# Optimization experiments

Hardware: AMD Instinct MI355X
Metric: run time of the kernel (lower is better)

The kernel has to match this reference:

```python
import jax, jax.numpy as jnp
import numpy as np

K = 1  # BaseSnapFunction.k default

def setup_inputs() -> dict:
    key = jax.random.key(0)
    k1, k2 = jax.random.split(key)
    B, S, D = 4, 2048, 1024
    C, N = 16, 2048          # num_codebooks, num_codes
    x = jax.random.normal(k1, (B, S, D), dtype=jnp.float32)
    codebook = jax.random.normal(k2, (C, N, D // C), dtype=jnp.float32)
    return {"x": x, "codebook": codebook}

def reference(x, codebook):
    B, S, D = x.shape
    C, N, sub = codebook.shape
    xr = x.reshape(B, S, C, sub)                      # split dim into C chunks
    # squared euclidean distance (monotone in true distance -> same argmin)
    dots = jnp.einsum('bscd,cnd->bscn', xr, codebook)  # [B,S,C,N]
    xsq = jnp.sum(xr * xr, axis=-1)                    # [B,S,C]
    cbsq = jnp.sum(codebook * codebook, axis=-1)       # [C,N]
    d2 = xsq[..., None] - 2.0 * dots + cbsq[None, None]
    idx = jnp.argmin(d2, axis=-1)                      # [B,S,C], k=1 topk of -dist
    # gather per-codebook features and concat chunks back to dim
    quant = codebook[jnp.arange(C)[None, None, :], idx]  # [B,S,C,sub]
    out = quant.reshape(B, S, D) / K
    return out
```

## Files before the change

### kernel.cpp

```cpp
#include <hip/hip_runtime.h>

constexpr int BS    = 8192;
constexpr int CCH   = 16;
constexpr int NCODE = 2048;

using s16x8 = __attribute__((ext_vector_type(8))) short;
using f32x4 = __attribute__((ext_vector_type(4))) float;


__device__ __forceinline__ unsigned short bf16_rne(float v) {
    unsigned u = __float_as_uint(v);
    return (unsigned short)((u + 0x7fffu + ((u >> 16) & 1u)) >> 16);
}
__device__ __forceinline__ void split1(float v, unsigned short& h, unsigned short& l) {
    h = bf16_rne(v);
    const float hf = __uint_as_float((unsigned)h << 16);
    l = bf16_rne(v - hf);
}
__device__ __forceinline__ void split4(float4 v, ushort4& h, ushort4& l) {
    split1(v.x, h.x, l.x); split1(v.y, h.y, l.y);
    split1(v.z, h.z, l.z); split1(v.w, h.w, l.w);
}
__device__ __forceinline__ unsigned enc_f(float s) {
    unsigned u = __float_as_uint(s);
    return (u & 0x80000000u) ? ~u : (u | 0x80000000u);
}

__device__ __forceinline__ s16x8 ldfrag(const char* buf, int row, int ke) {
    return *(const s16x8*)(buf + row * 128 + ((((ke >> 3) ^ row) & 7) * 16));
}

__device__ __forceinline__ void gload16(const void* g, void* l) {
    __builtin_amdgcn_global_load_lds(
        (const __attribute__((address_space(1))) void*)g,
        (__attribute__((address_space(3))) void*)l, 16, 0, 0);
}

__device__ __forceinline__ void merge2(float& b1, int& bi, float& b2,
                                       float ob1, int obi, float ob2) {
    b2 = fminf(fminf(b2, ob2), fmaxf(b1, ob1));
    if (ob1 < b1 || (ob1 == b1 && obi < bi)) { b1 = ob1; bi = obi; }
}

__global__ void cbsq_kernel(const float* __restrict__ cb, float* __restrict__ cbsq,
                            float* __restrict__ cmax)
{
    const int g = blockIdx.x * 256 + threadIdx.x;
    const float4* cg = (const float4*)cb;
    float s = 0.f;
#pragma unroll
    for (int q = 0; q < 16; ++q) {
        float4 v = cg[(size_t)g * 16 + q];
        s = fmaf(v.x, v.x, s); s = fmaf(v.y, v.y, s);
        s = fmaf(v.z, v.z, s); s = fmaf(v.w, v.w, s);
    }
    cbsq[g] = s;
    atomicMax((unsigned*)cmax, __float_as_uint(s));
}

__global__ void presplit_cb(const float* __restrict__ cb,
                            unsigned short* __restrict__ cbh,
                            unsigned short* __restrict__ cbl)
{
    const int g = blockIdx.x * 256 + threadIdx.x;
    const float4 v = ((const float4*)cb)[g];
    ushort4 h, l; split4(v, h, l);
    ((ushort4*)cbh)[g] = h;
    ((ushort4*)cbl)[g] = l;
}

__global__ __launch_bounds__(256, 2)
void vq_fp32_fallback(const float* __restrict__ x, const float* __restrict__ cb,
                      float* __restrict__ out)
{
    __shared__ __align__(16) char smraw[65536];
    float4 (*xs)[128] = reinterpret_cast<float4(*)[128]>(smraw);
    float4 (*cs)[128] = reinterpret_cast<float4(*)[128]>(smraw + 32768);
    float  (*rs)[128] = reinterpret_cast<float(*)[128]>(smraw);
    int    (*ri)[128] = reinterpret_cast<int(*)[128]>(smraw + 8192);
    int    *bfin      = reinterpret_cast<int*>(smraw + 16384);

    const int tid = threadIdx.x, tx = tid & 15, ty = tid >> 4;
    const int c = blockIdx.y, mbase = blockIdx.x * 128;
    const float4* xg = (const float4*)x;
    const float4* cg = (const float4*)cb;
    {
        const int k4 = tid & 15, mrow0 = tid >> 4;
#pragma unroll
        for (int i = 0; i < 8; ++i) {
            const int m = i * 16 + mrow0;
            xs[k4][m] = xg[(size_t)(mbase + m) * 256 + c * 16 + k4];
        }
    }
    float best[8]; int bidx[8];
#pragma unroll
    for (int ii = 0; ii < 8; ++ii) { best[ii] = 3.4e38f; bidx[ii] = 0; }
    for (int nt = 0; nt < 16; ++nt) {
        __syncthreads();
        {
            const int k4 = tid & 15, nrow0 = tid >> 4;
#pragma unroll
            for (int i = 0; i < 8; ++i) {
                const int n = i * 16 + nrow0;
                cs[k4][n] = cg[((size_t)c * NCODE + nt * 128 + n) * 16 + k4];
            }
        }
        __syncthreads();
        float acc[8][8], csq[8];
#pragma unroll
        for (int ii = 0; ii < 8; ++ii)
#pragma unroll
            for (int jj = 0; jj < 8; ++jj) acc[ii][jj] = 0.f;
#pragma unroll
        for (int jj = 0; jj < 8; ++jj) csq[jj] = 0.f;
#pragma unroll 2
        for (int k4 = 0; k4 < 16; ++k4) {
            float4 xv[8], cv[8];
#pragma unroll
            for (int ii = 0; ii < 8; ++ii) xv[ii] = xs[k4][tx + 16 * ii];
#pragma unroll
            for (int jj = 0; jj < 8; ++jj) cv[jj] = cs[k4][ty + 16 * jj];
#pragma unroll
            for (int jj = 0; jj < 8; ++jj) {
                csq[jj] = fmaf(cv[jj].x, cv[jj].x, csq[jj]);
                csq[jj] = fmaf(cv[jj].y, cv[jj].y, csq[jj]);
                csq[jj] = fmaf(cv[jj].z, cv[jj].z, csq[jj]);
                csq[jj] = fmaf(cv[jj].w, cv[jj].w, csq[jj]);
            }
#pragma unroll
            for (int ii = 0; ii < 8; ++ii)
#pragma unroll
                for (int jj = 0; jj < 8; ++jj) {
                    acc[ii][jj] = fmaf(xv[ii].x, cv[jj].x, acc[ii][jj]);
                    acc[ii][jj] = fmaf(xv[ii].y, cv[jj].y, acc[ii][jj]);
                    acc[ii][jj] = fmaf(xv[ii].z, cv[jj].z, acc[ii][jj]);
                    acc[ii][jj] = fmaf(xv[ii].w, cv[jj].w, acc[ii][jj]);
                }
        }
#pragma unroll
        for (int jj = 0; jj < 8; ++jj) {
            const int n = nt * 128 + ty + 16 * jj;
#pragma unroll
            for (int ii = 0; ii < 8; ++ii) {
                const float s = fmaf(-2.f, acc[ii][jj], csq[jj]);
                if (s < best[ii]) { best[ii] = s; bidx[ii] = n; }
            }
        }
    }
    __syncthreads();
#pragma unroll
    for (int ii = 0; ii < 8; ++ii) {
        const int m = tx + 16 * ii;
        rs[ty][m] = best[ii]; ri[ty][m] = bidx[ii];
    }
    __syncthreads();
    if (tid < 128) {
        float b = rs[0][tid]; int bi = ri[0][tid];
#pragma unroll
        for (int j = 1; j < 16; ++j) {
            const float s = rs[j][tid]; const int i2 = ri[j][tid];
            if (s < b || (s == b && i2 < bi)) { b = s; bi = i2; }
        }
        bfin[tid] = bi;
    }
    __syncthreads();
    {
        float4* og = (float4*)out;
#pragma unroll
        for (int i = 0; i < 8; ++i) {
            const int flat = i * 256 + tid, m = flat >> 4, q = flat & 15;
            og[(size_t)(mbase + m) * 256 + c * 16 + q] =
                cg[((size_t)c * NCODE + bfin[m]) * 16 + q];
        }
    }
}

template<bool PRESPLIT>
__global__ __launch_bounds__(256, 2)
void pass1(const float* __restrict__ x, const float* __restrict__ cb,
           const unsigned short* __restrict__ cbh, const unsigned short* __restrict__ cbl,
           const float* __restrict__ cbsq, const float* __restrict__ cmax,
           float* __restrict__ out, int* __restrict__ bcnt, int* __restrict__ bwl,
           unsigned long long* __restrict__ pbest)
{
    __shared__ __align__(1024) char sm[65536];
    const int tid  = threadIdx.x;
    const int lane = tid & 63, wv = tid >> 6;
    const int l15  = lane & 15, quad = lane >> 4;
    const int c = blockIdx.y, mbase = blockIdx.x * 128;
    const float4* xg = (const float4*)x;
    const float4* cg = (const float4*)cb;
    const float cmaxs = sqrtf(*cmax);
    const int cwb = (wv & 1) * 64, tkb = (wv >> 1) * 64;

    int tdec[4], ndec[4];
    {
        char* calV = sm;
        char* calO = sm + 16384;
#pragma unroll
        for (int i = 0; i < 8; ++i) {
            const int flat = i * 256 + tid, row = flat >> 4, f4c = flat & 15;
            const int off = row * 128 + ((((f4c >> 1) ^ row) & 7) * 16) + (f4c & 1) * 8;
            const unsigned short hv = bf16_rne((float)(row & 15));
            const unsigned short ho = bf16_rne(1.0f);
            ushort4 v4 = {hv, hv, hv, hv}, o4 = {ho, ho, ho, ho};
            *(ushort4*)(calV + off) = v4;
            *(ushort4*)(calO + off) = o4;
        }
        __syncthreads();
        const int ke = quad * 8;
        const s16x8 aV = ldfrag(calV, cwb + l15, ke);
        const s16x8 aO = ldfrag(calO, cwb + l15, ke);
        const s16x8 bV = ldfrag(calV, tkb + l15, ke);
        const s16x8 bO = ldfrag(calO, tkb + l15, ke);
        f32x4 z; z[0] = z[1] = z[2] = z[3] = 0.f;
        const f32x4 at = __builtin_amdgcn_mfma_f32_16x16x32_bf16(aO, bV, z, 0, 0, 0);
        const f32x4 an = __builtin_amdgcn_mfma_f32_16x16x32_bf16(aV, bO, z, 0, 0, 0);
#pragma unroll
        for (int r = 0; r < 4; ++r) {
            tdec[r] = ((int)(at[r] + 0.5f) >> 5) & 15;
            ndec[r] = ((int)(an[r] + 0.5f) >> 5) & 15;
        }
        __syncthreads();
    }

    char* xs_hi = sm;
    char* xs_lo = sm + 16384;
    {
        float4 xf[8];
#pragma unroll
        for (int i = 0; i < 8; ++i) {
            const int flat = i * 256 + tid;
            xf[i] = xg[(size_t)(mbase + (flat >> 4)) * 256 + c * 16 + (flat & 15)];
        }
#pragma unroll
        for (int i = 0; i < 8; ++i) {
            const int flat = i * 256 + tid, row = flat >> 4, f4c = flat & 15;
            ushort4 h, l; split4(xf[i], h, l);
            const int off = row * 128 + ((((f4c >> 1) ^ row) & 7) * 16) + (f4c & 1) * 8;
            *(ushort4*)(xs_hi + off) = h;
            *(ushort4*)(xs_lo + off) = l;
        }
    }
    __syncthreads();

    s16x8 bhf[4][2], blf[4][2];
#pragma unroll
    for (int jt = 0; jt < 4; ++jt)
#pragma unroll
        for (int ks = 0; ks < 2; ++ks) {
            const int rowt = tkb + jt * 16 + l15;
            const int ke = ks * 32 + quad * 8;
            bhf[jt][ks] = ldfrag(xs_hi, rowt, ke);
            blf[jt][ks] = ldfrag(xs_lo, rowt, ke);
        }

    float4 pf[8];
    uint4  ph[4], pl[4];
    if (PRESPLIT) {
        const uint4* sh = (const uint4*)(cbh + (size_t)c * NCODE * 64);
        const uint4* sl = (const uint4*)(cbl + (size_t)c * NCODE * 64);
#pragma unroll
        for (int i = 0; i < 4; ++i) {
            const int flat = i * 256 + tid;
            ph[i] = sh[flat]; pl[i] = sl[flat];
        }
    } else {
        const float4* src = cg + (size_t)c * NCODE * 16;
#pragma unroll
        for (int i = 0; i < 8; ++i) {
            const int flat = i * 256 + tid;
            pf[i] = src[(size_t)(flat >> 4) * 16 + (flat & 15)];
        }
    }

    float s1[4][4], s2[4][4]; int i1[4][4];
#pragma unroll
    for (int jt = 0; jt < 4; ++jt)
#pragma unroll
        for (int r = 0; r < 4; ++r) { s1[jt][r] = 3.4e38f; s2[jt][r] = 3.4e38f; i1[jt][r] = 0; }

    for (int nt = 0; nt < 16; ++nt) {
        char* chi = (nt & 1) ? sm : sm + 32768;
        char* clo = chi + 16384;
        if (PRESPLIT) {
#pragma unroll
            for (int i = 0; i < 4; ++i) {
                const int flat = i * 256 + tid;
                const int row = flat >> 3, ch = flat & 7;
                const int phys = (ch ^ row) & 7;
                *(uint4*)(chi + row * 128 + phys * 16) = ph[i];
                *(uint4*)(clo + row * 128 + phys * 16) = pl[i];
            }
        } else {
#pragma unroll
            for (int i = 0; i < 8; ++i) {
                const int flat = i * 256 + tid, row = flat >> 4, f4c = flat & 15;
                ushort4 h, l; split4(pf[i], h, l);
                const int off = row * 128 + ((((f4c >> 1) ^ row) & 7) * 16) + (f4c & 1) * 8;
                *(ushort4*)(chi + off) = h;
                *(ushort4*)(clo + off) = l;
            }
        }
        __syncthreads();
        if (nt < 15) {
            if (PRESPLIT) {
                const uint4* sh = (const uint4*)(cbh + ((size_t)c * NCODE + (nt + 1) * 128) * 64);
                const uint4* sl = (const uint4*)(cbl + ((size_t)c * NCODE + (nt + 1) * 128) * 64);
#pragma unroll
                for (int i = 0; i < 4; ++i) {
                    const int flat = i * 256 + tid;
                    ph[i] = sh[flat]; pl[i] = sl[flat];
                }
            } else {
                const float4* src = cg + ((size_t)c * NCODE + (nt + 1) * 128) * 16;
#pragma unroll
                for (int i = 0; i < 8; ++i) {
                    const int flat = i * 256 + tid;
                    pf[i] = src[(size_t)(flat >> 4) * 16 + (flat & 15)];
                }
            }
        }
        const float* cbn = cbsq + c * NCODE + nt * 128;
        float csqv[4][4];
#pragma unroll
        for (int mt = 0; mt < 4; ++mt)
#pragma unroll
            for (int r = 0; r < 4; ++r)
                csqv[mt][r] = cbn[cwb + mt * 16 + ndec[r]];

#pragma unroll
        for (int mt = 0; mt < 4; ++mt) {
            f32x4 accj[4];
#pragma unroll
            for (int jt = 0; jt < 4; ++jt)
#pragma unroll
                for (int e = 0; e < 4; ++e) accj[jt][e] = 0.f;
#pragma unroll
            for (int ks = 0; ks < 2; ++ks) {
                const int ke = ks * 32 + quad * 8;
                const int rowc = cwb + mt * 16 + l15;
                const s16x8 ah = ldfrag(chi, rowc, ke);
                const s16x8 al = ldfrag(clo, rowc, ke);
#pragma unroll
                for (int jt = 0; jt < 4; ++jt) {
                    accj[jt] = __builtin_amdgcn_mfma_f32_16x16x32_bf16(ah, bhf[jt][ks], accj[jt], 0, 0, 0);
                    accj[jt] = __builtin_amdgcn_mfma_f32_16x16x32_bf16(ah, blf[jt][ks], accj[jt], 0, 0, 0);
                    accj[jt] = __builtin_amdgcn_mfma_f32_16x16x32_bf16(al, bhf[jt][ks], accj[jt], 0, 0, 0);
                }
            }
#pragma unroll
            for (int jt = 0; jt < 4; ++jt)
#pragma unroll
                for (int r = 0; r < 4; ++r) {
                    const float s = fmaf(-2.f, accj[jt][r], csqv[mt][r]);
                    const int n = nt * 128 + cwb + mt * 16 + ndec[r];
                    const bool lt = s < s1[jt][r];
                    s2[jt][r] = fminf(s2[jt][r], fmaxf(s, s1[jt][r]));
                    i1[jt][r] = lt ? n : i1[jt][r];
                    s1[jt][r] = fminf(s1[jt][r], s);
                }
        }
    }

    __syncthreads();
    float* s1a = (float*)sm;
    int*   i1a = (int*)(sm + 16384);
    float* s2a = (float*)(sm + 32768);
    float* sm_part = (float*)(sm + 49152);
    int*   bfin    = (int*)(sm + 57344);
#pragma unroll
    for (int jt = 0; jt < 4; ++jt)
#pragma unroll
        for (int r = 0; r < 4; ++r) {
            const int tok = tkb + jt * 16 + tdec[r];
            const int idx = tok * 32 + (wv & 1) * 16 + ndec[r];
            s1a[idx] = s1[jt][r]; i1a[idx] = i1[jt][r]; s2a[idx] = s2[jt][r];
        }
    {
        const float4* src = xg + (size_t)mbase * 256 + c * 16;
#pragma unroll
        for (int i = 0; i < 8; ++i) {
            const int flat = i * 256 + tid, row = flat >> 4, f4c = flat & 15;
            const float4 v = src[(size_t)row * 256 + f4c];
            sm_part[row * 16 + f4c] = v.x * v.x + v.y * v.y + v.z * v.z + v.w * v.w;
        }
    }
    __syncthreads();
    if (tid < 128) {
        float b1 = 3.4e38f, b2 = 3.4e38f; int bi = 0;
#pragma unroll 4
        for (int e = 0; e < 32; ++e) {
            const float se = s1a[tid * 32 + e];
            const int   ie = i1a[tid * 32 + e];
            const float s2e = s2a[tid * 32 + e];
            if (se < b1 || (se == b1 && ie < bi)) { b2 = fminf(b2, b1); b1 = se; bi = ie; }
            else b2 = fminf(b2, se);
            b2 = fminf(b2, s2e);
        }
        float xsq = 0.f;
#pragma unroll
        for (int q = 0; q < 16; ++q) xsq += sm_part[tid * 16 + q];
        const float eps = 3e-4f + 2e-4f * sqrtf(xsq) * cmaxs;
        bfin[tid] = bi;
        if (b2 - b1 <= 2.f * eps) {
            const int slot = atomicAdd(&bcnt[c], 1);
            bwl[c * 8192 + slot] = mbase + tid;
            pbest[c * 8192 + slot] = ~0ULL;
        }
    }
    __syncthreads();
    {
        float4* og = (float4*)out;
#pragma unroll
        for (int i = 0; i < 8; ++i) {
            const int flat = i * 256 + tid, m = flat >> 4, q = flat & 15;
            og[(size_t)(mbase + m) * 256 + c * 16 + q] =
                cg[((size_t)c * NCODE + bfin[m]) * 16 + q];
        }
    }
}

__global__ __launch_bounds__(256, 2)
void pass1_gl(const float* __restrict__ x, const float* __restrict__ cb,
              const unsigned short* __restrict__ cbh, const unsigned short* __restrict__ cbl,
              const float* __restrict__ cbsq, const float* __restrict__ cmax,
              float* __restrict__ out, int* __restrict__ bcnt, int* __restrict__ bwl,
              unsigned long long* __restrict__ pbest)
{
    __shared__ __align__(1024) char sm[65536];
    const int tid  = threadIdx.x;
    const int lane = tid & 63, wv = tid >> 6;
    const int l15  = lane & 15, quad = lane >> 4;
    const int c = blockIdx.y, mbase = blockIdx.x * 128;
    const float4* xg = (const float4*)x;
    const float4* cg = (const float4*)cb;
    const float cmaxs = sqrtf(*cmax);
    const int cwb = (wv & 1) * 64, tkb = (wv >> 1) * 64;

    char* bufA = sm;
    char* bufB = sm + 32768;

    const int lanebyte = ((lane >> 3) << 7) | ((((lane & 7) ^ (lane >> 3)) & 7) << 4);
    const char* srcH = (const char*)cbh + (size_t)c * NCODE * 128;
    const char* srcL = (const char*)cbl + (size_t)c * NCODE * 128;
    const int wchunk = wv * 4096;

#pragma unroll
    for (int j = 0; j < 4; ++j) {
        const int o = wchunk + j * 1024;
        gload16(srcH + o + lanebyte, bufB + o);
        gload16(srcL + o + lanebyte, bufB + 16384 + o);
    }
    float4 xf[8];
#pragma unroll
    for (int i = 0; i < 8; ++i) {
        const int flat = i * 256 + tid;
        xf[i] = xg[(size_t)(mbase + (flat >> 4)) * 256 + c * 16 + (flat & 15)];
    }

    int tdec[4], ndec[4];
    {
        const short one = (short)bf16_rne(1.0f);
        const short val = (short)bf16_rne((float)l15);
        s16x8 aV, aO;
#pragma unroll
        for (int e = 0; e < 8; ++e) { aV[e] = val; aO[e] = one; }
        f32x4 z; z[0] = z[1] = z[2] = z[3] = 0.f;
        const f32x4 at = __builtin_amdgcn_mfma_f32_16x16x32_bf16(aO, aV, z, 0, 0, 0);
        const f32x4 an = __builtin_amdgcn_mfma_f32_16x16x32_bf16(aV, aO, z, 0, 0, 0);
#pragma unroll
        for (int r = 0; r < 4; ++r) {
            tdec[r] = ((int)(at[r] + 0.5f) >> 5) & 15;
            ndec[r] = ((int)(an[r] + 0.5f) >> 5) & 15;
        }
    }

    float p8[8];
#pragma unroll
    for (int i = 0; i < 8; ++i) {
        const int flat = i * 256 + tid, row = flat >> 4, f4c = flat & 15;
        ushort4 h, l; split4(xf[i], h, l);
        const int off = row * 128 + ((((f4c >> 1) ^ row) & 7) * 16) + (f4c & 1) * 8;
        *(ushort4*)(bufA + off) = h;
        *(ushort4*)(bufA + 16384 + off) = l;
        p8[i] = xf[i].x * xf[i].x + xf[i].y * xf[i].y + xf[i].z * xf[i].z + xf[i].w * xf[i].w;
    }
    __syncthreads();

    s16x8 bhf[4][2], blf[4][2];
#pragma unroll
    for (int jt = 0; jt < 4; ++jt)
#pragma unroll
        for (int ks = 0; ks < 2; ++ks) {
            const int rowt = tkb + jt * 16 + l15;
            const int ke = ks * 32 + quad * 8;
            bhf[jt][ks] = ldfrag(bufA, rowt, ke);
            blf[jt][ks] = ldfrag(bufA + 16384, rowt, ke);
        }
    __syncthreads();

    float s1[4][4], s2[4][4]; int i1[4][4];
#pragma unroll
    for (int jt = 0; jt < 4; ++jt)
#pragma unroll
        for (int r = 0; r < 4; ++r) { s1[jt][r] = 3.4e38f; s2[jt][r] = 3.4e38f; i1[jt][r] = 0; }

    for (int nt = 0; nt < 16; ++nt) {
        char* chi = (nt & 1) ? bufA : bufB;
        char* clo = chi + 16384;

        const float* cbn = cbsq + c * NCODE + nt * 128;
        float csqv[4][4];
#pragma unroll
        for (int mt = 0; mt < 4; ++mt)
#pragma unroll
            for (int r = 0; r < 4; ++r)
                csqv[mt][r] = cbn[cwb + mt * 16 + ndec[r]];
        asm volatile("" ::: "memory");

        if (nt < 15) {
            char* nh = (nt & 1) ? bufB : bufA;
            const char* th = srcH + (size_t)(nt + 1) * 16384;
            const char* tl = srcL + (size_t)(nt + 1) * 16384;
#pragma unroll
            for (int j = 0; j < 4; ++j) {
                const int o = wchunk + j * 1024;
                gload16(th + o + lanebyte, nh + o);
                gload16(tl + o + lanebyte, nh + 16384 + o);
            }
        }

#pragma unroll
        for (int mt = 0; mt < 4; ++mt) {
            f32x4 accj[4];
#pragma unroll
            for (int jt = 0; jt < 4; ++jt)
#pragma unroll
                for (int e = 0; e < 4; ++e) accj[jt][e] = 0.f;
#pragma unroll
            for (int ks = 0; ks < 2; ++ks) {
                const int ke = ks * 32 + quad * 8;
                const int rowc = cwb + mt * 16 + l15;
                const s16x8 ah = ldfrag(chi, rowc, ke);
                const s16x8 al = ldfrag(clo, rowc, ke);
#pragma unroll
                for (int jt = 0; jt < 4; ++jt) {
                    accj[jt] = __builtin_amdgcn_mfma_f32_16x16x32_bf16(ah, bhf[jt][ks], accj[jt], 0, 0, 0);
                    accj[jt] = __builtin_amdgcn_mfma_f32_16x16x32_bf16(ah, blf[jt][ks], accj[jt], 0, 0, 0);
                    accj[jt] = __builtin_amdgcn_mfma_f32_16x16x32_bf16(al, bhf[jt][ks], accj[jt], 0, 0, 0);
                }
            }
#pragma unroll
            for (int jt = 0; jt < 4; ++jt)
#pragma unroll
                for (int r = 0; r < 4; ++r) {
                    const float s = fmaf(-2.f, accj[jt][r], csqv[mt][r]);
                    const int n = nt * 128 + cwb + mt * 16 + ndec[r];
                    const bool lt = s < s1[jt][r];
                    s2[jt][r] = fminf(s2[jt][r], fmaxf(s, s1[jt][r]));
                    i1[jt][r] = lt ? n : i1[jt][r];
                    s1[jt][r] = fminf(s1[jt][r], s);
                }
        }
        __syncthreads();
    }

    float* s1h = (float*)sm;
    int*   i1h = (int*)  (sm + 1024);
    float* s2h = (float*)(sm + 2048);
    float* xsq_l = (float*)(sm + 3072);
    int*   bfin  = (int*)  (sm + 3584);

#pragma unroll
    for (int jt = 0; jt < 4; ++jt) {
        float b1 = s1[jt][0], b2 = s2[jt][0]; int bi = i1[jt][0];
#pragma unroll
        for (int r = 1; r < 4; ++r)
            merge2(b1, bi, b2, s1[jt][r], i1[jt][r], s2[jt][r]);
#pragma unroll
        for (int m = 16; m <= 32; m <<= 1) {
            const float ob1 = __shfl_xor(b1, m);
            const int   obi = __shfl_xor(bi, m);
            const float ob2 = __shfl_xor(b2, m);
            merge2(b1, bi, b2, ob1, obi, ob2);
        }
        if (quad == 0) {
            const int tok = tkb + jt * 16 + tdec[0];
            s1h[tok * 2 + (wv & 1)] = b1;
            i1h[tok * 2 + (wv & 1)] = bi;
            s2h[tok * 2 + (wv & 1)] = b2;
        }
    }
#pragma unroll
    for (int i = 0; i < 8; ++i) {
        float v = p8[i];
        v += __shfl_xor(v, 1); v += __shfl_xor(v, 2);
        v += __shfl_xor(v, 4); v += __shfl_xor(v, 8);
        if (l15 == 0) xsq_l[i * 16 + (tid >> 4)] = v;
    }
    __syncthreads();
    if (tid < 128) {
        float b1 = s1h[tid * 2], b2 = s2h[tid * 2]; int bi = i1h[tid * 2];
        merge2(b1, bi, b2, s1h[tid * 2 + 1], i1h[tid * 2 + 1], s2h[tid * 2 + 1]);
        const float xsq = xsq_l[tid];
        const float eps = 3e-4f + 2e-4f * sqrtf(xsq) * cmaxs;
        bfin[tid] = bi;
        if (b2 - b1 <= 2.f * eps) {
            const int slot = atomicAdd(&bcnt[c], 1);
            bwl[c * 8192 + slot] = mbase + tid;
            pbest[c * 8192 + slot] = ~0ULL;
        }
    }
    __syncthreads();
    {
        float4* og = (float4*)out;
#pragma unroll
        for (int i = 0; i < 8; ++i) {
            const int flat = i * 256 + tid, m = flat >> 4, q = flat & 15;
            og[(size_t)(mbase + m) * 256 + c * 16 + q] =
                cg[((size_t)c * NCODE + bfin[m]) * 16 + q];
        }
    }
}

__global__ __launch_bounds__(256, 2)
void pass2_nt(const float* __restrict__ x, const float* __restrict__ cb,
              const int* __restrict__ bcnt, const int* __restrict__ bwl,
              unsigned long long* __restrict__ pbest)
{
    __shared__ __align__(16) char smraw[65536];
    __shared__ int toks[128];
    float4 (*xs)[128] = reinterpret_cast<float4(*)[128]>(smraw);
    float4 (*cs)[128] = reinterpret_cast<float4(*)[128]>(smraw + 32768);
    float  (*rs)[128] = reinterpret_cast<float(*)[128]>(smraw);
    int    (*ri)[128] = reinterpret_cast<int(*)[128]>(smraw + 8192);

    const int c = blockIdx.y, ntb = blockIdx.x;
    const int cnt = bcnt[c];
    if (cnt == 0) return;
    const int tid = threadIdx.x, tx = tid & 15, ty = tid >> 4;
    const float4* xg = (const float4*)x;
    const float4* cg = (const float4*)cb;

    {
        const int k4 = tid & 15, nrow0 = tid >> 4;
#pragma unroll
        for (int i = 0; i < 8; ++i) {
            const int n = i * 16 + nrow0;
            cs[k4][n] = cg[((size_t)c * NCODE + ntb * 128 + n) * 16 + k4];
        }
    }

    for (int g0 = 0; g0 < cnt; g0 += 128) {
        __syncthreads();
        if (tid < 128) {
            const int e = g0 + tid;
            toks[tid] = bwl[c * 8192 + (e < cnt ? e : g0)];
        }
        __syncthreads();
        {
            const int k4 = tid & 15, mrow0 = tid >> 4;
#pragma unroll
            for (int i = 0; i < 8; ++i) {
                const int m = i * 16 + mrow0;
                xs[k4][m] = xg[(size_t)toks[m] * 256 + c * 16 + k4];
            }
        }
        __syncthreads();
        float acc[8][8], csq[8];
#pragma unroll
        for (int ii = 0; ii < 8; ++ii)
#pragma unroll
            for (int jj = 0; jj < 8; ++jj) acc[ii][jj] = 0.f;
#pragma unroll
        for (int jj = 0; jj < 8; ++jj) csq[jj] = 0.f;
#pragma unroll 2
        for (int k4 = 0; k4 < 16; ++k4) {
            float4 xv[8], cv[8];
#pragma unroll
            for (int ii = 0; ii < 8; ++ii) xv[ii] = xs[k4][tx + 16 * ii];
#pragma unroll
            for (int jj = 0; jj < 8; ++jj) cv[jj] = cs[k4][ty + 16 * jj];
#pragma unroll
            for (int jj = 0; jj < 8; ++jj) {
                csq[jj] = fmaf(cv[jj].x, cv[jj].x, csq[jj]);
                csq[jj] = fmaf(cv[jj].y, cv[jj].y, csq[jj]);
                csq[jj] = fmaf(cv[jj].z, cv[jj].z, csq[jj]);
                csq[jj] = fmaf(cv[jj].w, cv[jj].w, csq[jj]);
            }
#pragma unroll
            for (int ii = 0; ii < 8; ++ii)
#pragma unroll
                for (int jj = 0; jj < 8; ++jj) {
                    acc[ii][jj] = fmaf(xv[ii].x, cv[jj].x, acc[ii][jj]);
                    acc[ii][jj] = fmaf(xv[ii].y, cv[jj].y, acc[ii][jj]);
                    acc[ii][jj] = fmaf(xv[ii].z, cv[jj].z, acc[ii][jj]);
                    acc[ii][jj] = fmaf(xv[ii].w, cv[jj].w, acc[ii][jj]);
                }
        }
        float best[8]; int bidx[8];
#pragma unroll
        for (int ii = 0; ii < 8; ++ii) { best[ii] = 3.4e38f; bidx[ii] = 0; }
#pragma unroll
        for (int jj = 0; jj < 8; ++jj) {
            const int n = ntb * 128 + ty + 16 * jj;
#pragma unroll
            for (int ii = 0; ii < 8; ++ii) {
                const float s = fmaf(-2.f, acc[ii][jj], csq[jj]);
                if (s < best[ii]) { best[ii] = s; bidx[ii] = n; }
            }
        }
        __syncthreads();
#pragma unroll
        for (int ii = 0; ii < 8; ++ii) {
            const int m = tx + 16 * ii;
            rs[ty][m] = best[ii]; ri[ty][m] = bidx[ii];
        }
        __syncthreads();
        if (tid < 128 && g0 + tid < cnt) {
            float b = rs[0][tid]; int bi = ri[0][tid];
#pragma unroll
            for (int j = 1; j < 16; ++j) {
                const float s = rs[j][tid]; const int i2 = ri[j][tid];
                if (s < b || (s == b && i2 < bi)) { b = s; bi = i2; }
            }
            const unsigned long long pk =
                ((unsigned long long)enc_f(b) << 32) | (unsigned)bi;
            atomicMin(&pbest[c * 8192 + g0 + tid], pk);
        }
    }
}

__global__ void pass3(const float* __restrict__ cb, float* __restrict__ out,
                      const int* __restrict__ bcnt, const int* __restrict__ bwl,
                      const unsigned long long* __restrict__ pbest)
{
    const int c = blockIdx.y;
    const int cnt = bcnt[c];
    const float4* cg = (const float4*)cb;
    float4* og = (float4*)out;
    const int q = threadIdx.x & 15;
    for (int e = blockIdx.x * 16 + (threadIdx.x >> 4); e < cnt; e += 64 * 16) {
        const int tok = bwl[c * 8192 + e];
        const unsigned n = (unsigned)(pbest[c * 8192 + e] & 0xFFFFFFFFull);
        og[(size_t)tok * 256 + c * 16 + q] = cg[((size_t)c * NCODE + n) * 16 + q];
    }
}

extern "C" void kernel_launch(void* const* d_in, const int* in_sizes, int n_in,
                              void* d_out, int out_size, void* d_ws, size_t ws_size,
                              hipStream_t stream)
{
    const float* x  = (const float*)d_in[0];
    const float* cb = (const float*)d_in[1];
    float* out      = (float*)d_out;

    if (ws_size < (size_t)(2u << 20)) {
        dim3 grid(BS / 128, CCH);
        vq_fp32_fallback<<<grid, 256, 0, stream>>>(x, cb, out);
        return;
    }
    char* ws = (char*)d_ws;
    float* cbsq = (float*)ws;
    float* cmax = (float*)(ws + 131072);
    int*   bcnt = (int*)(ws + 131076);
    int*   bwl  = (int*)(ws + 131328);
    unsigned long long* pbest = (unsigned long long*)(ws + 655616);
    unsigned short* cbh = (unsigned short*)(ws + (2u << 20));
    unsigned short* cbl = (unsigned short*)(ws + (6u << 20));

    hipMemsetAsync(ws + 131072, 0, 68, stream);
    cbsq_kernel<<<CCH * NCODE / 256, 256, 0, stream>>>(cb, cbsq, cmax);
    if (ws_size >= (size_t)(10u << 20)) {
        presplit_cb<<<2048, 256, 0, stream>>>(cb, cbh, cbl);
        pass1_gl<<<dim3(BS / 128, CCH), 256, 0, stream>>>(x, cb, cbh, cbl, cbsq, cmax, out, bcnt, bwl, pbest);
    } else {
        pass1<false><<<dim3(BS / 128, CCH), 256, 0, stream>>>(x, cb, nullptr, nullptr, cbsq, cmax, out, bcnt, bwl, pbest);
    }
    pass2_nt<<<dim3(16, CCH), 256, 0, stream>>>(x, cb, bcnt, bwl, pbest);
    pass3<<<dim3(64, CCH), 256, 0, stream>>>(cb, out, bcnt, bwl, pbest);
}
```

Measured before the change: 228.7 us.

## Fuse codebook prep kernels and split pass1 work across eight waves

Merges the codebook squared-norm kernel and the bf16 hi/lo presplit kernel into a single prep kernel that reads each float4 once and reduces the norms with lane shuffles, removing one launch and one full read of the codebook. The main pass1 kernel now runs 512 threads (8 waves) per block instead of 256. Each wave handles 32 codes instead of 64 and does half the loads, and the per-token best/second-best merge now spans four wave partitions. This raises parallelism per block and cuts per-thread register use, at the cost of more LDS reduction traffic and a possible occupancy limit from 64KB of shared memory per block.

Result: slower. 758.8 us (+231.8%).

```diff
diff --git a/kernel.cpp b/kernel.cpp
--- a/kernel.cpp
+++ b/kernel.cpp
@@ -42,31 +42,25 @@
     if (ob1 < b1 || (ob1 == b1 && obi < bi)) { b1 = ob1; bi = obi; }
 }
 
-__global__ void cbsq_kernel(const float* __restrict__ cb, float* __restrict__ cbsq,
-                            float* __restrict__ cmax)
-{
-    const int g = blockIdx.x * 256 + threadIdx.x;
-    const float4* cg = (const float4*)cb;
-    float s = 0.f;
-#pragma unroll
-    for (int q = 0; q < 16; ++q) {
-        float4 v = cg[(size_t)g * 16 + q];
-        s = fmaf(v.x, v.x, s); s = fmaf(v.y, v.y, s);
-        s = fmaf(v.z, v.z, s); s = fmaf(v.w, v.w, s);
-    }
-    cbsq[g] = s;
-    atomicMax((unsigned*)cmax, __float_as_uint(s));
-}
-
-__global__ void presplit_cb(const float* __restrict__ cb,
-                            unsigned short* __restrict__ cbh,
-                            unsigned short* __restrict__ cbl)
+template<bool SPLIT>
+__global__ void prep(const float* __restrict__ cb, float* __restrict__ cbsq,
+                     float* __restrict__ cmax,
+                     unsigned short* __restrict__ cbh, unsigned short* __restrict__ cbl)
 {
     const int g = blockIdx.x * 256 + threadIdx.x;
     const float4 v = ((const float4*)cb)[g];
-    ushort4 h, l; split4(v, h, l);
-    ((ushort4*)cbh)[g] = h;
-    ((ushort4*)cbl)[g] = l;
+    if (SPLIT) {
+        ushort4 h, l; split4(v, h, l);
+        ((ushort4*)cbh)[g] = h;
+        ((ushort4*)cbl)[g] = l;
+    }
+    float s = v.x * v.x + v.y * v.y + v.z * v.z + v.w * v.w;
+    s += __shfl_xor(s, 1); s += __shfl_xor(s, 2);
+    s += __shfl_xor(s, 4); s += __shfl_xor(s, 8);
+    if ((threadIdx.x & 15) == 0) {
+        cbsq[g >> 4] = s;
+        atomicMax((unsigned*)cmax, __float_as_uint(s));
+    }
 }
 
 __global__ __launch_bounds__(256, 2)
@@ -421,12 +415,12 @@
     }
 }
 
-__global__ __launch_bounds__(256, 2)
-void pass1_gl(const float* __restrict__ x, const float* __restrict__ cb,
-              const unsigned short* __restrict__ cbh, const unsigned short* __restrict__ cbl,
-              const float* __restrict__ cbsq, const float* __restrict__ cmax,
-              float* __restrict__ out, int* __restrict__ bcnt, int* __restrict__ bwl,
-              unsigned long long* __restrict__ pbest)
+__global__ __launch_bounds__(512, 4)
+void pass1_gl8(const float* __restrict__ x, const float* __restrict__ cb,
+               const unsigned short* __restrict__ cbh, const unsigned short* __restrict__ cbl,
+               const float* __restrict__ cbsq, const float* __restrict__ cmax,
+               float* __restrict__ out, int* __restrict__ bcnt, int* __restrict__ bwl,
+               unsigned long long* __restrict__ pbest)
 {
     __shared__ __align__(1024) char sm[65536];
     const int tid  = threadIdx.x;
@@ -436,7 +430,8 @@
     const float4* xg = (const float4*)x;
     const float4* cg = (const float4*)cb;
     const float cmaxs = sqrtf(*cmax);
-    const int cwb = (wv & 1) * 64, tkb = (wv >> 1) * 64;
+    const int cwb = (wv & 3) * 32;
+    const int tkb = (wv >> 2) * 64;
 
     char* bufA = sm;
     char* bufB = sm + 32768;
@@ -444,18 +439,18 @@
     const int lanebyte = ((lane >> 3) << 7) | ((((lane & 7) ^ (lane >> 3)) & 7) << 4);
     const char* srcH = (const char*)cbh + (size_t)c * NCODE * 128;
     const char* srcL = (const char*)cbl + (size_t)c * NCODE * 128;
-    const int wchunk = wv * 4096;
-
-#pragma unroll
-    for (int j = 0; j < 4; ++j) {
+    const int wchunk = wv * 2048;
+
+#pragma unroll
+    for (int j = 0; j < 2; ++j) {
         const int o = wchunk + j * 1024;
         gload16(srcH + o + lanebyte, bufB + o);
         gload16(srcL + o + lanebyte, bufB + 16384 + o);
     }
-    float4 xf[8];
-#pragma unroll
-    for (int i = 0; i < 8; ++i) {
-        const int flat = i * 256 + tid;
+    float4 xf[4];
+#pragma unroll
+    for (int i = 0; i < 4; ++i) {
+        const int flat = i * 512 + tid;
         xf[i] = xg[(size_t)(mbase + (flat >> 4)) * 256 + c * 16 + (flat & 15)];
     }
 
@@ -476,15 +471,15 @@
         }
     }
 
-    float p8[8];
-#pragma unroll
-    for (int i = 0; i < 8; ++i) {
-        const int flat = i * 256 + tid, row = flat >> 4, f4c = flat & 15;
+    float p4[4];
+#pragma unroll
+    for (int i = 0; i < 4; ++i) {
+        const int flat = i * 512 + tid, row = flat >> 4, f4c = flat & 15;
         ushort4 h, l; split4(xf[i], h, l);
         const int off = row * 128 + ((((f4c >> 1) ^ row) & 7) * 16) + (f4c & 1) * 8;
         *(ushort4*)(bufA + off) = h;
         *(ushort4*)(bufA + 16384 + off) = l;
-        p8[i] = xf[i].x * xf[i].x + xf[i].y * xf[i].y + xf[i].z * xf[i].z + xf[i].w * xf[i].w;
+        p4[i] = xf[i].x * xf[i].x + xf[i].y * xf[i].y + xf[i].z * xf[i].z + xf[i].w * xf[i].w;
     }
     __syncthreads();
 
@@ -511,9 +506,9 @@
         char* clo = chi + 16384;
 
         const float* cbn = cbsq + c * NCODE + nt * 128;
-        float csqv[4][4];
-#pragma unroll
-        for (int mt = 0; mt < 4; ++mt)
+        float csqv[2][4];
+#pragma unroll
+        for (int mt = 0; mt < 2; ++mt)
 #pragma unroll
             for (int r = 0; r < 4; ++r)
                 csqv[mt][r] = cbn[cwb + mt * 16 + ndec[r]];
@@ -524,7 +519,7 @@
             const char* th = srcH + (size_t)(nt + 1) * 16384;
             const char* tl = srcL + (size_t)(nt + 1) * 16384;
 #pragma unroll
-            for (int j = 0; j < 4; ++j) {
+            for (int j = 0; j < 2; ++j) {
                 const int o = wchunk + j * 1024;
                 gload16(th + o + lanebyte, nh + o);
                 gload16(tl + o + lanebyte, nh + 16384 + o);
@@ -532,7 +527,7 @@
         }
 
 #pragma unroll
-        for (int mt = 0; mt < 4; ++mt) {
+        for (int mt = 0; mt < 2; ++mt) {
             f32x4 accj[4];
 #pragma unroll
             for (int jt = 0; jt < 4; ++jt)
@@ -567,10 +562,10 @@
     }
 
     float* s1h = (float*)sm;
-    int*   i1h = (int*)  (sm + 1024);
-    float* s2h = (float*)(sm + 2048);
-    float* xsq_l = (float*)(sm + 3072);
-    int*   bfin  = (int*)  (sm + 3584);
+    int*   i1h = (int*)  (sm + 2048);
+    float* s2h = (float*)(sm + 4096);
+    float* xsq_l = (float*)(sm + 6144);
+    int*   bfin  = (int*)  (sm + 6656);
 
 #pragma unroll
     for (int jt = 0; jt < 4; ++jt) {
@@ -587,22 +582,24 @@
         }
         if (quad == 0) {
             const int tok = tkb + jt * 16 + tdec[0];
-            s1h[tok * 2 + (wv & 1)] = b1;
-            i1h[tok * 2 + (wv & 1)] = bi;
-            s2h[tok * 2 + (wv & 1)] = b2;
-        }
-    }
-#pragma unroll
-    for (int i = 0; i < 8; ++i) {
-        float v = p8[i];
+            s1h[tok * 4 + (wv & 3)] = b1;
+            i1h[tok * 4 + (wv & 3)] = bi;
+            s2h[tok * 4 + (wv & 3)] = b2;
+        }
+    }
+#pragma unroll
+    for (int i = 0; i < 4; ++i) {
+        float v = p4[i];
         v += __shfl_xor(v, 1); v += __shfl_xor(v, 2);
         v += __shfl_xor(v, 4); v += __shfl_xor(v, 8);
-        if (l15 == 0) xsq_l[i * 16 + (tid >> 4)] = v;
+        if (l15 == 0) xsq_l[i * 32 + (tid >> 4)] = v;
     }
     __syncthreads();
     if (tid < 128) {
-        float b1 = s1h[tid * 2], b2 = s2h[tid * 2]; int bi = i1h[tid * 2];
-        merge2(b1, bi, b2, s1h[tid * 2 + 1], i1h[tid * 2 + 1], s2h[tid * 2 + 1]);
+        float b1 = s1h[tid * 4], b2 = s2h[tid * 4]; int bi = i1h[tid * 4];
+#pragma unroll
+        for (int q = 1; q < 4; ++q)
+            merge2(b1, bi, b2, s1h[tid * 4 + q], i1h[tid * 4 + q], s2h[tid * 4 + q]);
         const float xsq = xsq_l[tid];
         const float eps = 3e-4f + 2e-4f * sqrtf(xsq) * cmaxs;
         bfin[tid] = bi;
@@ -616,8 +613,8 @@
     {
         float4* og = (float4*)out;
 #pragma unroll
-        for (int i = 0; i < 8; ++i) {
-            const int flat = i * 256 + tid, m = flat >> 4, q = flat & 15;
+        for (int i = 0; i < 4; ++i) {
+            const int flat = i * 512 + tid, m = flat >> 4, q = flat & 15;
             og[(size_t)(mbase + m) * 256 + c * 16 + q] =
                 cg[((size_t)c * NCODE + bfin[m]) * 16 + q];
         }
@@ -771,11 +768,11 @@
     unsigned short* cbl = (unsigned short*)(ws + (6u << 20));
 
     hipMemsetAsync(ws + 131072, 0, 68, stream);
-    cbsq_kernel<<<CCH * NCODE / 256, 256, 0, stream>>>(cb, cbsq, cmax);
     if (ws_size >= (size_t)(10u << 20)) {
-        presplit_cb<<<2048, 256, 0, stream>>>(cb, cbh, cbl);
-        pass1_gl<<<dim3(BS / 128, CCH), 256, 0, stream>>>(x, cb, cbh, cbl, cbsq, cmax, out, bcnt, bwl, pbest);
+        prep<true><<<2048, 256, 0, stream>>>(cb, cbsq, cmax, cbh, cbl);
+        pass1_gl8<<<dim3(BS / 128, CCH), 512, 0, stream>>>(x, cb, cbh, cbl, cbsq, cmax, out, bcnt, bwl, pbest);
     } else {
+        prep<false><<<2048, 256, 0, stream>>>(cb, cbsq, cmax, nullptr, nullptr);
         pass1<false><<<dim3(BS / 128, CCH), 256, 0, stream>>>(x, cb, nullptr, nullptr, cbsq, cmax, out, bcnt, bwl, pbest);
     }
     pass2_nt<<<dim3(16, CCH), 256, 0, stream>>>(x, cb, bcnt, bwl, pbest);
```

## Fuse codebook norm and bf16 split prep; stage norms in LDS; use med3 for runner-up

Applied to the files above, without the earlier changes.

Merges the codebook squared-norm kernel and the bf16 hi/lo presplit kernel into one prep kernel. It reduces each row's norm with shuffles across 16 lanes and issues one atomicMax per row instead of one per thread. In pass1_gl, the per-codec norms are loaded once into LDS via global_load_lds, replacing per-tile scattered global loads. The runner-up distance update now uses v_med3_f32. This saves a kernel launch and global latency in the inner loop, but raises LDS use to 72KB per block, which could lower occupancy below 2 blocks per CU.

Result: slower. 301.0 us (+31.6%).

```diff
diff --git a/kernel.cpp b/kernel.cpp
--- a/kernel.cpp
+++ b/kernel.cpp
@@ -25,6 +25,11 @@
     unsigned u = __float_as_uint(s);
     return (u & 0x80000000u) ? ~u : (u | 0x80000000u);
 }
+__device__ __forceinline__ float med3f(float a, float b, float c) {
+    float d;
+    asm("v_med3_f32 %0, %1, %2, %3" : "=v"(d) : "v"(a), "v"(b), "v"(c));
+    return d;
+}
 
 __device__ __forceinline__ s16x8 ldfrag(const char* buf, int row, int ke) {
     return *(const s16x8*)(buf + row * 128 + ((((ke >> 3) ^ row) & 7) * 16));
@@ -42,31 +47,25 @@
     if (ob1 < b1 || (ob1 == b1 && obi < bi)) { b1 = ob1; bi = obi; }
 }
 
-__global__ void cbsq_kernel(const float* __restrict__ cb, float* __restrict__ cbsq,
-                            float* __restrict__ cmax)
-{
-    const int g = blockIdx.x * 256 + threadIdx.x;
-    const float4* cg = (const float4*)cb;
-    float s = 0.f;
-#pragma unroll
-    for (int q = 0; q < 16; ++q) {
-        float4 v = cg[(size_t)g * 16 + q];
-        s = fmaf(v.x, v.x, s); s = fmaf(v.y, v.y, s);
-        s = fmaf(v.z, v.z, s); s = fmaf(v.w, v.w, s);
-    }
-    cbsq[g] = s;
-    atomicMax((unsigned*)cmax, __float_as_uint(s));
-}
-
-__global__ void presplit_cb(const float* __restrict__ cb,
-                            unsigned short* __restrict__ cbh,
-                            unsigned short* __restrict__ cbl)
+template<bool SPLIT>
+__global__ void prep(const float* __restrict__ cb, float* __restrict__ cbsq,
+                     float* __restrict__ cmax,
+                     unsigned short* __restrict__ cbh, unsigned short* __restrict__ cbl)
 {
     const int g = blockIdx.x * 256 + threadIdx.x;
     const float4 v = ((const float4*)cb)[g];
-    ushort4 h, l; split4(v, h, l);
-    ((ushort4*)cbh)[g] = h;
-    ((ushort4*)cbl)[g] = l;
+    if (SPLIT) {
+        ushort4 h, l; split4(v, h, l);
+        ((ushort4*)cbh)[g] = h;
+        ((ushort4*)cbl)[g] = l;
+    }
+    float s = v.x * v.x + v.y * v.y + v.z * v.z + v.w * v.w;
+    s += __shfl_xor(s, 1); s += __shfl_xor(s, 2);
+    s += __shfl_xor(s, 4); s += __shfl_xor(s, 8);
+    if ((threadIdx.x & 15) == 0) {
+        cbsq[g >> 4] = s;
+        atomicMax((unsigned*)cmax, __float_as_uint(s));
+    }
 }
 
 __global__ __launch_bounds__(256, 2)
@@ -428,7 +427,7 @@
               float* __restrict__ out, int* __restrict__ bcnt, int* __restrict__ bwl,
               unsigned long long* __restrict__ pbest)
 {
-    __shared__ __align__(1024) char sm[65536];
+    __shared__ __align__(1024) char sm[73728];
     const int tid  = threadIdx.x;
     const int lane = tid & 63, wv = tid >> 6;
     const int l15  = lane & 15, quad = lane >> 4;
@@ -440,6 +439,7 @@
 
     char* bufA = sm;
     char* bufB = sm + 32768;
+    float* csq_l = (float*)(sm + 65536);
 
     const int lanebyte = ((lane >> 3) << 7) | ((((lane & 7) ^ (lane >> 3)) & 7) << 4);
     const char* srcH = (const char*)cbh + (size_t)c * NCODE * 128;
@@ -451,6 +451,14 @@
         const int o = wchunk + j * 1024;
         gload16(srcH + o + lanebyte, bufB + o);
         gload16(srcL + o + lanebyte, bufB + 16384 + o);
+    }
+    {
+        const char* cq = (const char*)(cbsq + (size_t)c * NCODE);
+#pragma unroll
+        for (int j = 0; j < 2; ++j) {
+            const int o = wv * 2048 + j * 1024;
+            gload16(cq + o + lane * 16, (char*)csq_l + o);
+        }
     }
     float4 xf[8];
 #pragma unroll
@@ -510,15 +518,6 @@
         char* chi = (nt & 1) ? bufA : bufB;
         char* clo = chi + 16384;
 
-        const float* cbn = cbsq + c * NCODE + nt * 128;
-        float csqv[4][4];
-#pragma unroll
-        for (int mt = 0; mt < 4; ++mt)
-#pragma unroll
-            for (int r = 0; r < 4; ++r)
-                csqv[mt][r] = cbn[cwb + mt * 16 + ndec[r]];
-        asm volatile("" ::: "memory");
-
         if (nt < 15) {
             char* nh = (nt & 1) ? bufB : bufA;
             const char* th = srcH + (size_t)(nt + 1) * 16384;
@@ -530,6 +529,13 @@
                 gload16(tl + o + lanebyte, nh + 16384 + o);
             }
         }
+
+        float csqv[4][4];
+#pragma unroll
+        for (int mt = 0; mt < 4; ++mt)
+#pragma unroll
+            for (int r = 0; r < 4; ++r)
+                csqv[mt][r] = csq_l[nt * 128 + cwb + mt * 16 + ndec[r]];
 
 #pragma unroll
         for (int mt = 0; mt < 4; ++mt) {
@@ -558,7 +564,7 @@
                     const float s = fmaf(-2.f, accj[jt][r], csqv[mt][r]);
                     const int n = nt * 128 + cwb + mt * 16 + ndec[r];
                     const bool lt = s < s1[jt][r];
-                    s2[jt][r] = fminf(s2[jt][r], fmaxf(s, s1[jt][r]));
+                    s2[jt][r] = med3f(s, s1[jt][r], s2[jt][r]);
                     i1[jt][r] = lt ? n : i1[jt][r];
                     s1[jt][r] = fminf(s1[jt][r], s);
                 }
@@ -771,11 +777,11 @@
     unsigned short* cbl = (unsigned short*)(ws + (6u << 20));
 
     hipMemsetAsync(ws + 131072, 0, 68, stream);
-    cbsq_kernel<<<CCH * NCODE / 256, 256, 0, stream>>>(cb, cbsq, cmax);
     if (ws_size >= (size_t)(10u << 20)) {
-        presplit_cb<<<2048, 256, 0, stream>>>(cb, cbh, cbl);
+        prep<true><<<2048, 256, 0, stream>>>(cb, cbsq, cmax, cbh, cbl);
         pass1_gl<<<dim3(BS / 128, CCH), 256, 0, stream>>>(x, cb, cbh, cbl, cbsq, cmax, out, bcnt, bwl, pbest);
     } else {
+        prep<false><<<2048, 256, 0, stream>>>(cb, cbsq, cmax, nullptr, nullptr);
         pass1<false><<<dim3(BS / 128, CCH), 256, 0, stream>>>(x, cb, nullptr, nullptr, cbsq, cmax, out, bcnt, bwl, pbest);
     }
     pass2_nt<<<dim3(16, CCH), 256, 0, stream>>>(x, cb, bcnt, bwl, pbest);
```
